# Kernel optimization log

Hardware: AMD Instinct MI355X
Metric: run time of the kernel (lower is better)

## Reference

```python
import jax, jax.numpy as jnp
import numpy as np

U, I, D, B, E = 100000, 50000, 64, 4, 2000000

def setup_inputs() -> dict:
    key = jax.random.key(0)
    k1, k2, k3, k4, k5, k6, k7 = jax.random.split(key, 7)
    user_embedding = jax.random.normal(k1, (U, D), dtype=jnp.float32) * 0.1
    item_embedding = jax.random.normal(k2, (I, D), dtype=jnp.float32) * 0.1
    rows = jax.random.randint(k3, (B, E), 0, U, dtype=jnp.int32)
    cols = jax.random.randint(k4, (B, E), 0, I, dtype=jnp.int32)
    # normalized-adjacency-like small positive values
    vals = jax.random.uniform(k5, (B, E), dtype=jnp.float32) * 0.05
    u_w = jax.random.normal(k6, (D, D), dtype=jnp.float32) * (1.0 / np.sqrt(D))
    i_w = jax.random.normal(k7, (D, D), dtype=jnp.float32) * (1.0 / np.sqrt(D))
    return {"user_embedding": user_embedding, "item_embedding": item_embedding,
            "rows": rows, "cols": cols, "vals": vals, "u_w": u_w, "i_w": i_w}

def reference(user_embedding, item_embedding, rows, cols, vals, u_w, i_w):
    n_users = user_embedding.shape[0]
    n_items = item_embedding.shape[0]

    # per-behavior spmm: A @ item_emb -> [U, D]; AT @ user_emb -> [I, D]
    def spmm_user(r, c, v):
        return jax.ops.segment_sum(v[:, None] * item_embedding[c], r,
                                   num_segments=n_users)

    def spmm_item(r, c, v):
        return jax.ops.segment_sum(v[:, None] * user_embedding[r], c,
                                   num_segments=n_items)

    user_stack = jax.vmap(spmm_user)(rows, cols, vals)  # [B, U, D]
    item_stack = jax.vmap(spmm_item)(rows, cols, vals)  # [B, I, D]

    user_emb = jax.nn.sigmoid(jnp.mean(user_stack, axis=0) @ u_w)   # [U, D]
    item_emb = jax.nn.sigmoid(jnp.mean(item_stack, axis=0) @ i_w)   # [I, D]
    user_embs = jax.nn.sigmoid(jnp.einsum('bud,de->bue', user_stack, u_w))  # [B, U, D]
    item_embs = jax.nn.sigmoid(jnp.einsum('bid,de->bie', item_stack, i_w))  # [B, I, D]
    return user_emb, item_emb, user_embs, item_embs
```

## Files before the change

kernel.cpp:

```cpp
#include <hip/hip_runtime.h>

#define U_N 100000
#define I_N 50000
#define D_N 64
#define B_N 4
#define E_N 2000000

#define EDGES   (B_N * E_N)
#define NSC_U   (U_N / 8)
#define NSC_I   (I_N / 8)
#define CROW    12544
#define NBLK    256
#define EPB     (EDGES / NBLK)
#define CAP     1536
#define SC_T    13


__global__ __launch_bounds__(256) void precompW_kernel(
        const float* __restrict__ emb, const float* __restrict__ W,
        unsigned short* __restrict__ out16, int nrows) {
    __shared__ float Wl[4096];
    int t = threadIdx.x, w = t >> 6, lane = t & 63;
    for (int i = t; i < 4096; i += 256) Wl[i] = W[i];
    __syncthreads();
    int base = blockIdx.x * 32;
#pragma unroll
    for (int it = 0; it < 8; ++it) {
        int row = base + it * 4 + w;
        float x = (row < nrows) ? emb[row * 64 + lane] : 0.f;
        float y = 0.f;
#pragma unroll 8
        for (int d = 0; d < 64; ++d)
            y = fmaf(__shfl(x, d), Wl[d * 64 + lane], y);
        if (row < nrows) {
            unsigned u = __float_as_uint(y);
            u += 0x7FFFu + ((u >> 16) & 1u);
            out16[row * 64 + lane] = (unsigned short)(u >> 16);
        }
    }
}

__global__ __launch_bounds__(512) void bhist_kernel(const int* __restrict__ keys,
                                                    int nsc,
                                                    int* __restrict__ cnt) {
    __shared__ int h[CROW];
    for (int i = threadIdx.x; i < nsc; i += 512) h[i] = 0;
    __syncthreads();
    int lb = ((blockIdx.x & 7) << 5) | (blockIdx.x >> 3);
    int base = lb * EPB;
    for (int i = threadIdx.x; i < EPB; i += 512)
        atomicAdd(&h[keys[base + i] >> 3], 1);
    __syncthreads();
    int* row = cnt + (size_t)lb * CROW;
    for (int i = threadIdx.x; i < nsc; i += 512) row[i] = h[i];
}

__global__ __launch_bounds__(512) void scan_tot(const int* __restrict__ cnt,
                                                int nsc, int* __restrict__ cnt_ch) {
    int c = blockIdx.x * 512 + threadIdx.x;
    if (c >= nsc) return;
    int s = 0;
    for (int lb = 0; lb < NBLK; ++lb) s += cnt[(size_t)lb * CROW + c];
    cnt_ch[c] = s;
}

__global__ __launch_bounds__(1024) void scan_ex(const int* __restrict__ cnt_ch,
                                                int nsc, int* __restrict__ off_ch) {
    int t = threadIdx.x;
    int loc[SC_T]; int s = 0;
#pragma unroll
    for (int j = 0; j < SC_T; ++j) {
        int idx = t * SC_T + j;
        int c = (idx < nsc) ? cnt_ch[idx] : 0;
        loc[j] = s; s += c;
    }
    __shared__ int sm[1024];
    int mine = s; sm[t] = s; __syncthreads();
    for (int o = 1; o < 1024; o <<= 1) {
        int a = (t >= o) ? sm[t - o] : 0;
        __syncthreads(); sm[t] += a; __syncthreads();
    }
    int pre = sm[t] - mine;
#pragma unroll
    for (int j = 0; j < SC_T; ++j) {
        int idx = t * SC_T + j;
        if (idx < nsc) off_ch[idx] = pre + loc[j];
    }
}

__global__ __launch_bounds__(512) void scan_cur(int* __restrict__ cnt,
                                                const int* __restrict__ off_ch,
                                                int nsc) {
    int c = blockIdx.x * 512 + threadIdx.x;
    if (c >= nsc) return;
    int run = off_ch[c];
    for (int lb = 0; lb < NBLK; ++lb) {
        int v = cnt[(size_t)lb * CROW + c];
        cnt[(size_t)lb * CROW + c] = run;
        run += v;
    }
}

__global__ __launch_bounds__(512) void cplace_kernel(const int* __restrict__ keys,
                                                     const int* __restrict__ srcs,
                                                     const float* __restrict__ vals,
                                                     const int* __restrict__ cur_g,
                                                     int nsc,
                                                     uint2* __restrict__ pay) {
    __shared__ int cur[CROW];
    int lb = ((blockIdx.x & 7) << 5) | (blockIdx.x >> 3);
    const int* row = cur_g + (size_t)lb * CROW;
    for (int i = threadIdx.x; i < nsc; i += 512) cur[i] = row[i];
    __syncthreads();
    int base = lb * EPB;
    int b = lb >> 6;
    for (int i = threadIdx.x; i < EPB; i += 512) {
        int gi = base + i;
        int k = keys[gi];
        float v = vals[gi];
        int src = srcs[gi];
        int pos = atomicAdd(&cur[k >> 3], 1);
        pay[pos] = make_uint2(((unsigned)(((k & 7) << 2) | b) << 17) | (unsigned)src,
                              __float_as_uint(v));
    }
}

__global__ __launch_bounds__(512) void fused_kernel(
        const unsigned short* __restrict__ embW16,
        const int* __restrict__ off_ch,
        const int* __restrict__ cnt_ch,
        const uint2* __restrict__ pay,
        float* __restrict__ embs,
        float* __restrict__ mean_out,
        int nrows) {
    int g = blockIdx.x;
    int start = off_ch[g], n = cnt_ch[g];
    int t = threadIdx.x, w = t >> 6, lane = t & 63;

    __shared__ uint2 st2[CAP];
    __shared__ int c32[32];
    __shared__ int bstart[33];
    float* ys = (float*)st2;

    if (n <= CAP) {
        if (t < 32) c32[t] = 0;
        __syncthreads();
        for (int i = t; i < n; i += 512)
            atomicAdd(&c32[pay[start + i].x >> 17], 1);
        __syncthreads();
        if (t == 0) {
            int s = 0;
            for (int b2 = 0; b2 < 32; ++b2) {
                bstart[b2] = s; s += c32[b2]; c32[b2] = bstart[b2];
            }
            bstart[32] = s;
        }
        __syncthreads();
        for (int i = t; i < n; i += 512) {
            uint2 p = pay[start + i];
            int pos = atomicAdd(&c32[p.x >> 17], 1);
            st2[pos] = p;
        }
        __syncthreads();

        int qt = lane >> 4, ql = lane & 15;
        float4 a0, a1, a2, a3;
#define ACC_BIN(AQ, Q)                                                        \
        {                                                                     \
            int s0 = bstart[w * 4 + (Q)], s1 = bstart[w * 4 + (Q) + 1];       \
            AQ = make_float4(0.f, 0.f, 0.f, 0.f);                             \
            for (int j = s0; j < s1; j += 4) {                                \
                int idx = j + qt;                                             \
                int jj = idx < s1 ? idx : s1 - 1;                             \
                uint2 p = st2[jj];                                            \
                float v = (idx < s1) ? __uint_as_float(p.y) : 0.f;            \
                uint2 x = *((const uint2*)(embW16 +                           \
                              (size_t)(p.x & 0x1FFFFu) * 64) + ql);           \
                AQ.x = fmaf(v, __uint_as_float(x.x << 16), AQ.x);             \
                AQ.y = fmaf(v, __uint_as_float(x.x & 0xFFFF0000u), AQ.y);     \
                AQ.z = fmaf(v, __uint_as_float(x.y << 16), AQ.z);             \
                AQ.w = fmaf(v, __uint_as_float(x.y & 0xFFFF0000u), AQ.w);     \
            }                                                                 \
            AQ.x += __shfl_xor(AQ.x, 16); AQ.x += __shfl_xor(AQ.x, 32);       \
            AQ.y += __shfl_xor(AQ.y, 16); AQ.y += __shfl_xor(AQ.y, 32);       \
            AQ.z += __shfl_xor(AQ.z, 16); AQ.z += __shfl_xor(AQ.z, 32);       \
            AQ.w += __shfl_xor(AQ.w, 16); AQ.w += __shfl_xor(AQ.w, 32);       \
        }
        ACC_BIN(a0, 0)
        ACC_BIN(a1, 1)
        ACC_BIN(a2, 2)
        ACC_BIN(a3, 3)
#undef ACC_BIN
        if (qt == 0) {
            int row = g * 8 + w;
            float4 yq[4] = {a0, a1, a2, a3};
#pragma unroll
            for (int q = 0; q < 4; ++q) {
                float4 s4;
                s4.x = 1.f / (1.f + __expf(-yq[q].x));
                s4.y = 1.f / (1.f + __expf(-yq[q].y));
                s4.z = 1.f / (1.f + __expf(-yq[q].z));
                s4.w = 1.f / (1.f + __expf(-yq[q].w));
                *(float4*)&embs[((long long)q * nrows + row) * 64 + 4 * ql] = s4;
            }
            float4 m4;
            m4.x = 0.25f * (a0.x + a1.x + a2.x + a3.x);
            m4.y = 0.25f * (a0.y + a1.y + a2.y + a3.y);
            m4.z = 0.25f * (a0.z + a1.z + a2.z + a3.z);
            m4.w = 0.25f * (a0.w + a1.w + a2.w + a3.w);
            m4.x = 1.f / (1.f + __expf(-m4.x));
            m4.y = 1.f / (1.f + __expf(-m4.y));
            m4.z = 1.f / (1.f + __expf(-m4.z));
            m4.w = 1.f / (1.f + __expf(-m4.w));
            *(float4*)&mean_out[(long long)row * 64 + 4 * ql] = m4;
        }
    } else {
        for (int i = t; i < 2048; i += 512) ys[i] = 0.f;
        __syncthreads();
        for (int j = w; j < n; j += 8) {
            uint2 pv = pay[start + j];
            float x = __uint_as_float(
                (unsigned)embW16[(size_t)(pv.x & 0x1FFFFu) * 64 + lane] << 16);
            atomicAdd(&ys[(pv.x >> 17) * 64 + lane],
                      __uint_as_float(pv.y) * x);
        }
        __syncthreads();
        int row = g * 8 + w;
        float y[4];
#pragma unroll
        for (int q = 0; q < 4; ++q) {
            y[q] = ys[(w * 4 + q) * 64 + lane];
            embs[((long long)q * nrows + row) * 64 + lane] =
                1.f / (1.f + __expf(-y[q]));
        }
        float m = 0.25f * (y[0] + y[1] + y[2] + y[3]);
        mean_out[(long long)row * 64 + lane] = 1.f / (1.f + __expf(-m));
    }
}

__global__ void scatter_atomic_kernel(const float* __restrict__ user_emb,
                                      const float* __restrict__ item_emb,
                                      const int* __restrict__ rows,
                                      const int* __restrict__ cols,
                                      const float* __restrict__ vals,
                                      float* __restrict__ stack_u,
                                      float* __restrict__ stack_i) {
    long long tid = (long long)blockIdx.x * blockDim.x + threadIdx.x;
    long long e  = tid >> 4;
    int lane = (int)(tid & 15);
    if (e >= (long long)EDGES) return;
    int b = (int)(e / E_N);
    int r = rows[e];
    int c = cols[e];
    float v = vals[e];
    const float4* irow = (const float4*)(item_emb + (long long)c * D_N);
    const float4* urow = (const float4*)(user_emb + (long long)r * D_N);
    float4 iv = irow[lane];
    float4 uv = urow[lane];
    float* du = stack_u + ((long long)b * U_N + r) * D_N + lane * 4;
    float* di = stack_i + ((long long)b * I_N + c) * D_N + lane * 4;
    atomicAdd(du + 0, v * iv.x);
    atomicAdd(du + 1, v * iv.y);
    atomicAdd(du + 2, v * iv.z);
    atomicAdd(du + 3, v * iv.w);
    atomicAdd(di + 0, v * uv.x);
    atomicAdd(di + 1, v * uv.y);
    atomicAdd(di + 2, v * uv.z);
    atomicAdd(di + 3, v * uv.w);
}

template <int NROWS>
__global__ __launch_bounds__(64) void transform_kernel(
        float* __restrict__ stack,
        const float* __restrict__ W,
        float* __restrict__ mean_out) {
    const int row = blockIdx.x;
    const int j   = threadIdx.x;
    __shared__ float xs[B_N][D_N];
#pragma unroll
    for (int b = 0; b < B_N; ++b)
        xs[b][j] = stack[((long long)b * NROWS + row) * D_N + j];
    __syncthreads();
    float acc[B_N] = {0.f, 0.f, 0.f, 0.f};
#pragma unroll 8
    for (int d = 0; d < D_N; ++d) {
        float w = W[d * D_N + j];
#pragma unroll
        for (int b = 0; b < B_N; ++b)
            acc[b] += xs[b][d] * w;
    }
    float m = 0.25f * (acc[0] + acc[1] + acc[2] + acc[3]);
#pragma unroll
    for (int b = 0; b < B_N; ++b)
        stack[((long long)b * NROWS + row) * D_N + j] =
            1.0f / (1.0f + __expf(-acc[b]));
    mean_out[(long long)row * D_N + j] = 1.0f / (1.0f + __expf(-m));
}

extern "C" void kernel_launch(void* const* d_in, const int* in_sizes, int n_in,
                              void* d_out, int out_size, void* d_ws, size_t ws_size,
                              hipStream_t stream) {
    const float* user_emb = (const float*)d_in[0];
    const float* item_emb = (const float*)d_in[1];
    const int*   rows     = (const int*)  d_in[2];
    const int*   cols     = (const int*)  d_in[3];
    const float* vals     = (const float*)d_in[4];
    const float* u_w      = (const float*)d_in[5];
    const float* i_w      = (const float*)d_in[6];

    float* out = (float*)d_out;
    float* user_mean = out;
    float* item_mean = out + (long long)U_N * D_N;
    float* stack_u   = item_mean + (long long)I_N * D_N;
    float* stack_i   = stack_u + (long long)B_N * U_N * D_N;

    int* cnt    = (int*)d_ws;
    int* cnt_ch = cnt + (size_t)NBLK * CROW;
    int* off_ch = cnt_ch + CROW;
    uint2* pay  = (uint2*)(off_ch + CROW);
    unsigned short* userW16 = (unsigned short*)(pay + EDGES);
    unsigned short* itemW16 = userW16 + (size_t)U_N * D_N;
    size_t needed = ((size_t)NBLK * CROW + 2 * CROW) * 4 +
                    (size_t)EDGES * 8 + (size_t)(U_N + I_N) * D_N * 2;

    if (ws_size >= needed) {
        precompW_kernel<<<(I_N + 31) / 32, 256, 0, stream>>>(item_emb, u_w,
                                                             itemW16, I_N);
        precompW_kernel<<<(U_N + 31) / 32, 256, 0, stream>>>(user_emb, i_w,
                                                             userW16, U_N);
        bhist_kernel<<<NBLK, 512, 0, stream>>>(rows, NSC_U, cnt);
        scan_tot<<<(NSC_U + 511) / 512, 512, 0, stream>>>(cnt, NSC_U, cnt_ch);
        scan_ex<<<1, 1024, 0, stream>>>(cnt_ch, NSC_U, off_ch);
        scan_cur<<<(NSC_U + 511) / 512, 512, 0, stream>>>(cnt, off_ch, NSC_U);
        cplace_kernel<<<NBLK, 512, 0, stream>>>(rows, cols, vals, cnt, NSC_U, pay);
        fused_kernel<<<NSC_U, 512, 0, stream>>>(itemW16, off_ch, cnt_ch, pay,
                                                stack_u, user_mean, U_N);
        bhist_kernel<<<NBLK, 512, 0, stream>>>(cols, NSC_I, cnt);
        scan_tot<<<(NSC_I + 511) / 512, 512, 0, stream>>>(cnt, NSC_I, cnt_ch);
        scan_ex<<<1, 1024, 0, stream>>>(cnt_ch, NSC_I, off_ch);
        scan_cur<<<(NSC_I + 511) / 512, 512, 0, stream>>>(cnt, off_ch, NSC_I);
        cplace_kernel<<<NBLK, 512, 0, stream>>>(cols, rows, vals, cnt, NSC_I, pay);
        fused_kernel<<<NSC_I, 512, 0, stream>>>(userW16, off_ch, cnt_ch, pay,
                                                stack_i, item_mean, I_N);
    } else {
        size_t stack_bytes = sizeof(float) * (size_t)B_N * (U_N + I_N) * D_N;
        hipMemsetAsync(stack_u, 0, stack_bytes, stream);
        long long nthreads = (long long)EDGES * 16;
        int nblocks = (int)((nthreads + 255) / 256);
        scatter_atomic_kernel<<<nblocks, 256, 0, stream>>>(
            user_emb, item_emb, rows, cols, vals, stack_u, stack_i);
        transform_kernel<U_N><<<U_N, 64, 0, stream>>>(stack_u, u_w, user_mean);
        transform_kernel<I_N><<<I_N, 64, 0, stream>>>(stack_i, i_w, item_mean);
    }
}
```

Baseline: 996.3 us.

## Compress edge payload to 5 bytes and histograms to 16-bit counts

Edge payloads shrink from 8 bytes to a 4-byte word (15-bit bf16-like value plus 17-bit source index) and a separate 1-byte local-bin array. Per-block histograms and cursors are stored as 16-bit counts, with the block count doubled to 512 and threads per block raised to 1024. Placement now runs in two passes over halves of the chunk range so the shared cursor array fits. This cuts global traffic for the sort and fused-gather stages, at the cost of reading keys twice in placement and lower precision for the edge values.

```diff
diff --git a/kernel.cpp b/kernel.cpp
--- a/kernel.cpp
+++ b/kernel.cpp
@@ -9,10 +9,11 @@
 #define EDGES   (B_N * E_N)
 #define NSC_U   (U_N / 8)
 #define NSC_I   (I_N / 8)
-#define CROW    12544
-#define NBLK    256
+#define CROW    12512
+#define NBLK    512
 #define EPB     (EDGES / NBLK)
 #define CAP     1536
+#define HCAP    6272
 #define SC_T    13
 
 
@@ -40,27 +41,33 @@
     }
 }
 
-__global__ __launch_bounds__(512) void bhist_kernel(const int* __restrict__ keys,
-                                                    int nsc,
-                                                    int* __restrict__ cnt) {
-    __shared__ int h[CROW];
-    for (int i = threadIdx.x; i < nsc; i += 512) h[i] = 0;
+__global__ __launch_bounds__(1024) void bhist_kernel(const int* __restrict__ keys,
+                                                     int nsc,
+                                                     unsigned short* __restrict__ cnt16) {
+    __shared__ unsigned h[CROW / 2];
+    for (int i = threadIdx.x; i < CROW / 2; i += 1024) h[i] = 0;
     __syncthreads();
-    int lb = ((blockIdx.x & 7) << 5) | (blockIdx.x >> 3);
+    int lb = ((blockIdx.x & 7) << 6) | (blockIdx.x >> 3);
     int base = lb * EPB;
-    for (int i = threadIdx.x; i < EPB; i += 512)
-        atomicAdd(&h[keys[base + i] >> 3], 1);
+    for (int i = threadIdx.x; i < EPB; i += 1024) {
+        int rc = keys[base + i] >> 3;
+        atomicAdd(&h[rc >> 1], 1u << ((rc & 1) * 16));
+    }
     __syncthreads();
-    int* row = cnt + (size_t)lb * CROW;
-    for (int i = threadIdx.x; i < nsc; i += 512) row[i] = h[i];
-}
-
-__global__ __launch_bounds__(512) void scan_tot(const int* __restrict__ cnt,
-                                                int nsc, int* __restrict__ cnt_ch) {
-    int c = blockIdx.x * 512 + threadIdx.x;
+    unsigned short* row = cnt16 + (size_t)lb * CROW;
+    for (int i = threadIdx.x; i < CROW / 2; i += 1024) {
+        unsigned v = h[i];
+        row[2 * i]     = (unsigned short)(v & 0xFFFFu);
+        row[2 * i + 1] = (unsigned short)(v >> 16);
+    }
+}
+
+__global__ __launch_bounds__(1024) void scan_tot(const unsigned short* __restrict__ cnt16,
+                                                 int nsc, int* __restrict__ cnt_ch) {
+    int c = blockIdx.x * 1024 + threadIdx.x;
     if (c >= nsc) return;
     int s = 0;
-    for (int lb = 0; lb < NBLK; ++lb) s += cnt[(size_t)lb * CROW + c];
+    for (int lb = 0; lb < NBLK; ++lb) s += cnt16[(size_t)lb * CROW + c];
     cnt_ch[c] = s;
 }
 
@@ -88,40 +95,52 @@
     }
 }
 
-__global__ __launch_bounds__(512) void scan_cur(int* __restrict__ cnt,
-                                                const int* __restrict__ off_ch,
-                                                int nsc) {
-    int c = blockIdx.x * 512 + threadIdx.x;
+__global__ __launch_bounds__(1024) void scan_cur(const unsigned short* __restrict__ cnt16,
+                                                 unsigned short* __restrict__ cur16,
+                                                 int nsc) {
+    int c = blockIdx.x * 1024 + threadIdx.x;
     if (c >= nsc) return;
-    int run = off_ch[c];
+    int run = 0;
     for (int lb = 0; lb < NBLK; ++lb) {
-        int v = cnt[(size_t)lb * CROW + c];
-        cnt[(size_t)lb * CROW + c] = run;
-        run += v;
-    }
-}
-
-__global__ __launch_bounds__(512) void cplace_kernel(const int* __restrict__ keys,
-                                                     const int* __restrict__ srcs,
-                                                     const float* __restrict__ vals,
-                                                     const int* __restrict__ cur_g,
-                                                     int nsc,
-                                                     uint2* __restrict__ pay) {
-    __shared__ int cur[CROW];
-    int lb = ((blockIdx.x & 7) << 5) | (blockIdx.x >> 3);
-    const int* row = cur_g + (size_t)lb * CROW;
-    for (int i = threadIdx.x; i < nsc; i += 512) cur[i] = row[i];
-    __syncthreads();
+        cur16[(size_t)lb * CROW + c] = (unsigned short)run;
+        run += cnt16[(size_t)lb * CROW + c];
+    }
+}
+
+__global__ __launch_bounds__(1024) void cplace_kernel(const int* __restrict__ keys,
+                                                      const int* __restrict__ srcs,
+                                                      const float* __restrict__ vals,
+                                                      const int* __restrict__ off_ch,
+                                                      const unsigned short* __restrict__ cur16,
+                                                      int nsc, int half,
+                                                      unsigned* __restrict__ payK,
+                                                      unsigned char* __restrict__ payL) {
+    __shared__ int cur[HCAP];
+    int lb = ((blockIdx.x & 7) << 6) | (blockIdx.x >> 3);
     int base = lb * EPB;
-    int b = lb >> 6;
-    for (int i = threadIdx.x; i < EPB; i += 512) {
-        int gi = base + i;
-        int k = keys[gi];
-        float v = vals[gi];
-        int src = srcs[gi];
-        int pos = atomicAdd(&cur[k >> 3], 1);
-        pay[pos] = make_uint2(((unsigned)(((k & 7) << 2) | b) << 17) | (unsigned)src,
-                              __float_as_uint(v));
+    int b = lb >> 7;
+    const unsigned short* crow = cur16 + (size_t)lb * CROW;
+    for (int pass = 0; pass < 2; ++pass) {
+        int lo = pass * half;
+        int hi = lo + half; if (hi > nsc) hi = nsc;
+        int m = hi - lo;
+        for (int i = threadIdx.x; i < m; i += 1024)
+            cur[i] = off_ch[lo + i] + (int)crow[lo + i];
+        __syncthreads();
+        for (int i = threadIdx.x; i < EPB; i += 1024) {
+            int gi = base + i;
+            int k = keys[gi];
+            int chunk = k >> 3;
+            if (chunk >= lo && chunk < hi) {
+                unsigned u = __float_as_uint(vals[gi]);
+                u += 0x7FFFu + ((u >> 16) & 1u);
+                unsigned bf15 = (u >> 16) & 0x7FFFu;
+                int pos = atomicAdd(&cur[chunk - lo], 1);
+                payK[pos] = (bf15 << 17) | (unsigned)srcs[gi];
+                payL[pos] = (unsigned char)(((k & 7) << 2) | b);
+            }
+        }
+        __syncthreads();
     }
 }
 
@@ -129,7 +148,8 @@
         const unsigned short* __restrict__ embW16,
         const int* __restrict__ off_ch,
         const int* __restrict__ cnt_ch,
-        const uint2* __restrict__ pay,
+        const unsigned* __restrict__ payK,
+        const unsigned char* __restrict__ payL,
         float* __restrict__ embs,
         float* __restrict__ mean_out,
         int nrows) {
@@ -137,7 +157,7 @@
     int start = off_ch[g], n = cnt_ch[g];
     int t = threadIdx.x, w = t >> 6, lane = t & 63;
 
-    __shared__ uint2 st2[CAP];
+    __shared__ unsigned st2[2048];
     __shared__ int c32[32];
     __shared__ int bstart[33];
     float* ys = (float*)st2;
@@ -146,7 +166,7 @@
         if (t < 32) c32[t] = 0;
         __syncthreads();
         for (int i = t; i < n; i += 512)
-            atomicAdd(&c32[pay[start + i].x >> 17], 1);
+            atomicAdd(&c32[payL[start + i]], 1);
         __syncthreads();
         if (t == 0) {
             int s = 0;
@@ -157,9 +177,8 @@
         }
         __syncthreads();
         for (int i = t; i < n; i += 512) {
-            uint2 p = pay[start + i];
-            int pos = atomicAdd(&c32[p.x >> 17], 1);
-            st2[pos] = p;
+            int pos = atomicAdd(&c32[payL[start + i]], 1);
+            st2[pos] = payK[start + i];
         }
         __syncthreads();
 
@@ -172,10 +191,11 @@
             for (int j = s0; j < s1; j += 4) {                                \
                 int idx = j + qt;                                             \
                 int jj = idx < s1 ? idx : s1 - 1;                             \
-                uint2 p = st2[jj];                                            \
-                float v = (idx < s1) ? __uint_as_float(p.y) : 0.f;            \
+                unsigned p = st2[jj];                                         \
+                float v = (idx < s1)                                          \
+                    ? __uint_as_float((p & 0xFFFE0000u) >> 1) : 0.f;          \
                 uint2 x = *((const uint2*)(embW16 +                           \
-                              (size_t)(p.x & 0x1FFFFu) * 64) + ql);           \
+                              (size_t)(p & 0x1FFFFu) * 64) + ql);             \
                 AQ.x = fmaf(v, __uint_as_float(x.x << 16), AQ.x);             \
                 AQ.y = fmaf(v, __uint_as_float(x.x & 0xFFFF0000u), AQ.y);     \
                 AQ.z = fmaf(v, __uint_as_float(x.y << 16), AQ.z);             \
@@ -218,11 +238,12 @@
         for (int i = t; i < 2048; i += 512) ys[i] = 0.f;
         __syncthreads();
         for (int j = w; j < n; j += 8) {
-            uint2 pv = pay[start + j];
+            unsigned p = payK[start + j];
+            int local = payL[start + j];
+            float v = __uint_as_float((p & 0xFFFE0000u) >> 1);
             float x = __uint_as_float(
-                (unsigned)embW16[(size_t)(pv.x & 0x1FFFFu) * 64 + lane] << 16);
-            atomicAdd(&ys[(pv.x >> 17) * 64 + lane],
-                      __uint_as_float(pv.y) * x);
+                (unsigned)embW16[(size_t)(p & 0x1FFFFu) * 64 + lane] << 16);
+            atomicAdd(&ys[local * 64 + lane], v * x);
         }
         __syncthreads();
         int row = g * 8 + w;
@@ -314,34 +335,37 @@
     float* stack_u   = item_mean + (long long)I_N * D_N;
     float* stack_i   = stack_u + (long long)B_N * U_N * D_N;
 
-    int* cnt    = (int*)d_ws;
-    int* cnt_ch = cnt + (size_t)NBLK * CROW;
+    unsigned* payK = (unsigned*)d_ws;
+    unsigned char* payL = (unsigned char*)(payK + EDGES);
+    unsigned short* userW16 = (unsigned short*)(payL + (size_t)EDGES);
+    unsigned short* itemW16 = userW16 + (size_t)U_N * D_N;
+    unsigned short* cnt16 = itemW16 + (size_t)I_N * D_N;
+    unsigned short* cur16 = cnt16 + (size_t)NBLK * CROW;
+    int* cnt_ch = (int*)(cur16 + (size_t)NBLK * CROW);
     int* off_ch = cnt_ch + CROW;
-    uint2* pay  = (uint2*)(off_ch + CROW);
-    unsigned short* userW16 = (unsigned short*)(pay + EDGES);
-    unsigned short* itemW16 = userW16 + (size_t)U_N * D_N;
-    size_t needed = ((size_t)NBLK * CROW + 2 * CROW) * 4 +
-                    (size_t)EDGES * 8 + (size_t)(U_N + I_N) * D_N * 2;
+    size_t needed = ((char*)(off_ch + CROW)) - (char*)d_ws;
 
     if (ws_size >= needed) {
         precompW_kernel<<<(I_N + 31) / 32, 256, 0, stream>>>(item_emb, u_w,
                                                              itemW16, I_N);
         precompW_kernel<<<(U_N + 31) / 32, 256, 0, stream>>>(user_emb, i_w,
                                                              userW16, U_N);
-        bhist_kernel<<<NBLK, 512, 0, stream>>>(rows, NSC_U, cnt);
-        scan_tot<<<(NSC_U + 511) / 512, 512, 0, stream>>>(cnt, NSC_U, cnt_ch);
+        bhist_kernel<<<NBLK, 1024, 0, stream>>>(rows, NSC_U, cnt16);
+        scan_tot<<<(NSC_U + 1023) / 1024, 1024, 0, stream>>>(cnt16, NSC_U, cnt_ch);
         scan_ex<<<1, 1024, 0, stream>>>(cnt_ch, NSC_U, off_ch);
-        scan_cur<<<(NSC_U + 511) / 512, 512, 0, stream>>>(cnt, off_ch, NSC_U);
-        cplace_kernel<<<NBLK, 512, 0, stream>>>(rows, cols, vals, cnt, NSC_U, pay);
-        fused_kernel<<<NSC_U, 512, 0, stream>>>(itemW16, off_ch, cnt_ch, pay,
-                                                stack_u, user_mean, U_N);
-        bhist_kernel<<<NBLK, 512, 0, stream>>>(cols, NSC_I, cnt);
-        scan_tot<<<(NSC_I + 511) / 512, 512, 0, stream>>>(cnt, NSC_I, cnt_ch);
+        scan_cur<<<(NSC_U + 1023) / 1024, 1024, 0, stream>>>(cnt16, cur16, NSC_U);
+        cplace_kernel<<<NBLK, 1024, 0, stream>>>(rows, cols, vals, off_ch, cur16,
+                                                 NSC_U, NSC_U / 2, payK, payL);
+        fused_kernel<<<NSC_U, 512, 0, stream>>>(itemW16, off_ch, cnt_ch,
+                                                payK, payL, stack_u, user_mean, U_N);
+        bhist_kernel<<<NBLK, 1024, 0, stream>>>(cols, NSC_I, cnt16);
+        scan_tot<<<(NSC_I + 1023) / 1024, 1024, 0, stream>>>(cnt16, NSC_I, cnt_ch);
         scan_ex<<<1, 1024, 0, stream>>>(cnt_ch, NSC_I, off_ch);
-        scan_cur<<<(NSC_I + 511) / 512, 512, 0, stream>>>(cnt, off_ch, NSC_I);
-        cplace_kernel<<<NBLK, 512, 0, stream>>>(cols, rows, vals, cnt, NSC_I, pay);
-        fused_kernel<<<NSC_I, 512, 0, stream>>>(userW16, off_ch, cnt_ch, pay,
-                                                stack_i, item_mean, I_N);
+        scan_cur<<<(NSC_I + 1023) / 1024, 1024, 0, stream>>>(cnt16, cur16, NSC_I);
+        cplace_kernel<<<NBLK, 1024, 0, stream>>>(cols, rows, vals, off_ch, cur16,
+                                                 NSC_I, NSC_I / 2, payK, payL);
+        fused_kernel<<<NSC_I, 512, 0, stream>>>(userW16, off_ch, cnt_ch,
+                                                payK, payL, stack_i, item_mean, I_N);
     } else {
         size_t stack_bytes = sizeof(float) * (size_t)B_N * (U_N + I_N) * D_N;
         hipMemsetAsync(stack_u, 0, stack_bytes, stream);
```

Measured after the change: 1.025 ms. +2.8%, slower.

## Pack histogram counts into 16-bit words and widen sort-stage blocks

Applied to the files above, without the earlier changes.

The per-block bucket histogram is stored as 16-bit counts, two packed per shared-memory word, which halves the count-matrix traffic in the scan kernels. scan_cur now writes block-local 16-bit offsets, and cplace adds the global chunk offset when it loads them. The sort kernels move to 1024-thread blocks, and precompW broadcasts each row through shared memory instead of using shuffles. Each block sees about 31k edges, so a 16-bit count overflows only if one bucket gets more than 65535 of them, which uniform keys make very unlikely but skewed inputs could hit.

```diff
diff --git a/kernel.cpp b/kernel.cpp
--- a/kernel.cpp
+++ b/kernel.cpp
@@ -9,7 +9,7 @@
 #define EDGES   (B_N * E_N)
 #define NSC_U   (U_N / 8)
 #define NSC_I   (I_N / 8)
-#define CROW    12544
+#define CROW    12512
 #define NBLK    256
 #define EPB     (EDGES / NBLK)
 #define CAP     1536
@@ -20,19 +20,21 @@
         const float* __restrict__ emb, const float* __restrict__ W,
         unsigned short* __restrict__ out16, int nrows) {
     __shared__ float Wl[4096];
+    __shared__ float xs[4][64];
     int t = threadIdx.x, w = t >> 6, lane = t & 63;
     for (int i = t; i < 4096; i += 256) Wl[i] = W[i];
-    __syncthreads();
     int base = blockIdx.x * 32;
 #pragma unroll
     for (int it = 0; it < 8; ++it) {
         int row = base + it * 4 + w;
-        float x = (row < nrows) ? emb[row * 64 + lane] : 0.f;
-        float y = 0.f;
+        __syncthreads();
+        xs[w][lane] = (row < nrows) ? emb[row * 64 + lane] : 0.f;
+        __syncthreads();
+        if (row < nrows) {
+            float y = 0.f;
 #pragma unroll 8
-        for (int d = 0; d < 64; ++d)
-            y = fmaf(__shfl(x, d), Wl[d * 64 + lane], y);
-        if (row < nrows) {
+            for (int d = 0; d < 64; ++d)
+                y = fmaf(xs[w][d], Wl[d * 64 + lane], y);
             unsigned u = __float_as_uint(y);
             u += 0x7FFFu + ((u >> 16) & 1u);
             out16[row * 64 + lane] = (unsigned short)(u >> 16);
@@ -40,27 +42,32 @@
     }
 }
 
-__global__ __launch_bounds__(512) void bhist_kernel(const int* __restrict__ keys,
-                                                    int nsc,
-                                                    int* __restrict__ cnt) {
-    __shared__ int h[CROW];
-    for (int i = threadIdx.x; i < nsc; i += 512) h[i] = 0;
+__global__ __launch_bounds__(1024) void bhist_kernel(const int* __restrict__ keys,
+                                                     unsigned short* __restrict__ cnt16) {
+    __shared__ unsigned h[CROW / 2];
+    for (int i = threadIdx.x; i < CROW / 2; i += 1024) h[i] = 0;
     __syncthreads();
     int lb = ((blockIdx.x & 7) << 5) | (blockIdx.x >> 3);
     int base = lb * EPB;
-    for (int i = threadIdx.x; i < EPB; i += 512)
-        atomicAdd(&h[keys[base + i] >> 3], 1);
+    for (int i = threadIdx.x; i < EPB; i += 1024) {
+        int rc = keys[base + i] >> 3;
+        atomicAdd(&h[rc >> 1], 1u << ((rc & 1) * 16));
+    }
     __syncthreads();
-    int* row = cnt + (size_t)lb * CROW;
-    for (int i = threadIdx.x; i < nsc; i += 512) row[i] = h[i];
-}
-
-__global__ __launch_bounds__(512) void scan_tot(const int* __restrict__ cnt,
-                                                int nsc, int* __restrict__ cnt_ch) {
-    int c = blockIdx.x * 512 + threadIdx.x;
+    unsigned short* row = cnt16 + (size_t)lb * CROW;
+    for (int i = threadIdx.x; i < CROW / 2; i += 1024) {
+        unsigned v = h[i];
+        row[2 * i]     = (unsigned short)(v & 0xFFFFu);
+        row[2 * i + 1] = (unsigned short)(v >> 16);
+    }
+}
+
+__global__ __launch_bounds__(1024) void scan_tot(const unsigned short* __restrict__ cnt16,
+                                                 int nsc, int* __restrict__ cnt_ch) {
+    int c = blockIdx.x * 1024 + threadIdx.x;
     if (c >= nsc) return;
     int s = 0;
-    for (int lb = 0; lb < NBLK; ++lb) s += cnt[(size_t)lb * CROW + c];
+    for (int lb = 0; lb < NBLK; ++lb) s += cnt16[(size_t)lb * CROW + c];
     cnt_ch[c] = s;
 }
 
@@ -88,33 +95,34 @@
     }
 }
 
-__global__ __launch_bounds__(512) void scan_cur(int* __restrict__ cnt,
-                                                const int* __restrict__ off_ch,
-                                                int nsc) {
-    int c = blockIdx.x * 512 + threadIdx.x;
+__global__ __launch_bounds__(1024) void scan_cur(const unsigned short* __restrict__ cnt16,
+                                                 unsigned short* __restrict__ cur16,
+                                                 int nsc) {
+    int c = blockIdx.x * 1024 + threadIdx.x;
     if (c >= nsc) return;
-    int run = off_ch[c];
+    int run = 0;
     for (int lb = 0; lb < NBLK; ++lb) {
-        int v = cnt[(size_t)lb * CROW + c];
-        cnt[(size_t)lb * CROW + c] = run;
-        run += v;
-    }
-}
-
-__global__ __launch_bounds__(512) void cplace_kernel(const int* __restrict__ keys,
-                                                     const int* __restrict__ srcs,
-                                                     const float* __restrict__ vals,
-                                                     const int* __restrict__ cur_g,
-                                                     int nsc,
-                                                     uint2* __restrict__ pay) {
+        cur16[(size_t)lb * CROW + c] = (unsigned short)run;
+        run += cnt16[(size_t)lb * CROW + c];
+    }
+}
+
+__global__ __launch_bounds__(1024) void cplace_kernel(const int* __restrict__ keys,
+                                                      const int* __restrict__ srcs,
+                                                      const float* __restrict__ vals,
+                                                      const int* __restrict__ off_ch,
+                                                      const unsigned short* __restrict__ cur16,
+                                                      int nsc,
+                                                      uint2* __restrict__ pay) {
     __shared__ int cur[CROW];
     int lb = ((blockIdx.x & 7) << 5) | (blockIdx.x >> 3);
-    const int* row = cur_g + (size_t)lb * CROW;
-    for (int i = threadIdx.x; i < nsc; i += 512) cur[i] = row[i];
+    const unsigned short* crow = cur16 + (size_t)lb * CROW;
+    for (int i = threadIdx.x; i < nsc; i += 1024)
+        cur[i] = off_ch[i] + (int)crow[i];
     __syncthreads();
     int base = lb * EPB;
     int b = lb >> 6;
-    for (int i = threadIdx.x; i < EPB; i += 512) {
+    for (int i = threadIdx.x; i < EPB; i += 1024) {
         int gi = base + i;
         int k = keys[gi];
         float v = vals[gi];
@@ -314,32 +322,34 @@
     float* stack_u   = item_mean + (long long)I_N * D_N;
     float* stack_i   = stack_u + (long long)B_N * U_N * D_N;
 
-    int* cnt    = (int*)d_ws;
-    int* cnt_ch = cnt + (size_t)NBLK * CROW;
-    int* off_ch = cnt_ch + CROW;
-    uint2* pay  = (uint2*)(off_ch + CROW);
+    uint2* pay = (uint2*)d_ws;
     unsigned short* userW16 = (unsigned short*)(pay + EDGES);
     unsigned short* itemW16 = userW16 + (size_t)U_N * D_N;
-    size_t needed = ((size_t)NBLK * CROW + 2 * CROW) * 4 +
-                    (size_t)EDGES * 8 + (size_t)(U_N + I_N) * D_N * 2;
+    unsigned short* cnt16 = itemW16 + (size_t)I_N * D_N;
+    unsigned short* cur16 = cnt16 + (size_t)NBLK * CROW;
+    int* cnt_ch = (int*)(cur16 + (size_t)NBLK * CROW);
+    int* off_ch = cnt_ch + CROW;
+    size_t needed = ((char*)(off_ch + CROW)) - (char*)d_ws;
 
     if (ws_size >= needed) {
         precompW_kernel<<<(I_N + 31) / 32, 256, 0, stream>>>(item_emb, u_w,
                                                              itemW16, I_N);
         precompW_kernel<<<(U_N + 31) / 32, 256, 0, stream>>>(user_emb, i_w,
                                                              userW16, U_N);
-        bhist_kernel<<<NBLK, 512, 0, stream>>>(rows, NSC_U, cnt);
-        scan_tot<<<(NSC_U + 511) / 512, 512, 0, stream>>>(cnt, NSC_U, cnt_ch);
+        bhist_kernel<<<NBLK, 1024, 0, stream>>>(rows, cnt16);
+        scan_tot<<<(NSC_U + 1023) / 1024, 1024, 0, stream>>>(cnt16, NSC_U, cnt_ch);
         scan_ex<<<1, 1024, 0, stream>>>(cnt_ch, NSC_U, off_ch);
-        scan_cur<<<(NSC_U + 511) / 512, 512, 0, stream>>>(cnt, off_ch, NSC_U);
-        cplace_kernel<<<NBLK, 512, 0, stream>>>(rows, cols, vals, cnt, NSC_U, pay);
+        scan_cur<<<(NSC_U + 1023) / 1024, 1024, 0, stream>>>(cnt16, cur16, NSC_U);
+        cplace_kernel<<<NBLK, 1024, 0, stream>>>(rows, cols, vals, off_ch, cur16,
+                                                 NSC_U, pay);
         fused_kernel<<<NSC_U, 512, 0, stream>>>(itemW16, off_ch, cnt_ch, pay,
                                                 stack_u, user_mean, U_N);
-        bhist_kernel<<<NBLK, 512, 0, stream>>>(cols, NSC_I, cnt);
-        scan_tot<<<(NSC_I + 511) / 512, 512, 0, stream>>>(cnt, NSC_I, cnt_ch);
+        bhist_kernel<<<NBLK, 1024, 0, stream>>>(cols, cnt16);
+        scan_tot<<<(NSC_I + 1023) / 1024, 1024, 0, stream>>>(cnt16, NSC_I, cnt_ch);
         scan_ex<<<1, 1024, 0, stream>>>(cnt_ch, NSC_I, off_ch);
-        scan_cur<<<(NSC_I + 511) / 512, 512, 0, stream>>>(cnt, off_ch, NSC_I);
-        cplace_kernel<<<NBLK, 512, 0, stream>>>(cols, rows, vals, cnt, NSC_I, pay);
+        scan_cur<<<(NSC_I + 1023) / 1024, 1024, 0, stream>>>(cnt16, cur16, NSC_I);
+        cplace_kernel<<<NBLK, 1024, 0, stream>>>(cols, rows, vals, off_ch, cur16,
+                                                 NSC_I, pay);
         fused_kernel<<<NSC_I, 512, 0, stream>>>(userW16, off_ch, cnt_ch, pay,
                                                 stack_i, item_mean, I_N);
     } else {
```

Measured after the change: 906.1 us. 1.1x faster.
